# Kernel optimization log

Hardware: AMD Instinct MI355X
Metric: run time of the kernel (lower is better)

The kernel has to match this reference:

```python
import jax, jax.numpy as jnp
import numpy as np
from jax import lax

B, SQ, SK, D, K = 4, 2048, 2048, 1024, 3


def setup_inputs() -> dict:
    key = jax.random.key(0)
    ks = jax.random.split(key, 16)
    s = 0.02
    return {
        "query_hidden": jax.random.normal(ks[0], (B, SQ, D), jnp.float32),
        "memory_hidden": jax.random.normal(ks[1], (B, SK, D), jnp.float32),
        "attention_mask": jax.random.randint(ks[2], (SQ, SK), 0, 2).astype(bool),
        # Linear projections (torch: y = x @ W.T + b)
        "q_w": jax.random.normal(ks[3], (D, D), jnp.float32) * s,
        "q_b": jnp.zeros((D,), jnp.float32),
        "k_w": jax.random.normal(ks[4], (D, D), jnp.float32) * s,
        "k_b": jnp.zeros((D,), jnp.float32),
        "v_w": jax.random.normal(ks[5], (D, D), jnp.float32) * s,
        "v_b": jnp.zeros((D,), jnp.float32),
        "o_w": jax.random.normal(ks[6], (D, D), jnp.float32) * s,
        "o_b": jnp.zeros((D,), jnp.float32),
        # ConvTransform1D: depthwise conv kernels [D,1,K], bias [D], scalar gate
        "q_kernel": jax.random.normal(ks[7], (D, 1, K), jnp.float32) * s,
        "q_cbias": jnp.zeros((D,), jnp.float32),
        "q_gate": jnp.zeros((), jnp.float32),
        "k_kernel": jax.random.normal(ks[8], (D, 1, K), jnp.float32) * s,
        "k_cbias": jnp.zeros((D,), jnp.float32),
        "k_gate": jnp.zeros((), jnp.float32),
        "v_kernel": jax.random.normal(ks[9], (D, 1, K), jnp.float32) * s,
        "v_cbias": jnp.zeros((D,), jnp.float32),
        "v_gate": jnp.zeros((), jnp.float32),
    }


def _conv_transform(x, kernel, cbias, gate):
    """Gated depthwise 1D conv along seq: x + tanh(gate) * dwconv(x). x: [B,S,D]."""
    xc = jnp.transpose(x, (0, 2, 1))  # [B,D,S]
    y = lax.conv_general_dilated(
        xc, kernel, window_strides=(1,), padding="SAME",
        dimension_numbers=("NCH", "OIH", "NCH"), feature_group_count=x.shape[-1])
    y = y + cbias[None, :, None]
    return x + jnp.tanh(gate) * jnp.transpose(y, (0, 2, 1))


def reference(query_hidden, memory_hidden, attention_mask,
              q_w, q_b, k_w, k_b, v_w, v_b, o_w, o_b,
              q_kernel, q_cbias, q_gate,
              k_kernel, k_cbias, k_gate,
              v_kernel, v_cbias, v_gate):
    d_model = query_hidden.shape[-1]
    q = _conv_transform(query_hidden @ q_w.T + q_b, q_kernel, q_cbias, q_gate)
    k = _conv_transform(memory_hidden @ k_w.T + k_b, k_kernel, k_cbias, k_gate)
    v = _conv_transform(memory_hidden @ v_w.T + v_b, v_kernel, v_cbias, v_gate)
    # [B,Sq,Sk]
    logits = jnp.einsum("bqd,bkd->bqk", q, k) / jnp.sqrt(jnp.float32(d_model))
    mask = attention_mask[None, :, :]  # broadcast like torch unsqueeze(0)
    logits = jnp.where(mask, logits, jnp.finfo(logits.dtype).min)
    attn = jax.nn.softmax(logits, axis=-1)
    out = jnp.einsum("bqk,bkd->bqd", attn, v) @ o_w.T + o_b
    return out
```

## Files before the change

### kernel.cpp

```cpp
#include <hip/hip_runtime.h>
#include <cstdint>
#include <cstddef>


#define GLOBAL_AS __attribute__((address_space(1)))
#define LDS_AS    __attribute__((address_space(3)))

typedef _Float16 h8 __attribute__((ext_vector_type(8)));
typedef float    f4_t __attribute__((ext_vector_type(4)));
typedef unsigned short us8 __attribute__((ext_vector_type(8)));

__device__ __forceinline__ float bf2f(unsigned short u) {
    union { unsigned int i; float f; } x; x.i = ((unsigned int)u) << 16; return x.f;
}
__device__ __forceinline__ float rd(const void* p, long i, int isBf) {
    return isBf ? bf2f(((const unsigned short*)p)[i]) : ((const float*)p)[i];
}

struct Probe16 { const unsigned short* p[16]; int n[16]; };

__global__ void k_probes(Probe16 a, const unsigned int* __restrict__ mask,
                         int* __restrict__ flags) {
    if (blockIdx.x < 16) {
        __shared__ int cnt;
        if (threadIdx.x == 0) cnt = 0;
        __syncthreads();
        const unsigned short* s = a.p[blockIdx.x];
        const int n = a.n[blockIdx.x];
        int bad = 0;
        for (int i = threadIdx.x; i < n; i += 256) {
            int e = (s[i] >> 7) & 0xFF;
            if (e >= 0x8F || (e > 0 && e <= 0x60)) bad++;
        }
        atomicAdd(&cnt, bad);
        __syncthreads();
        if (threadIdx.x == 0) flags[blockIdx.x] = (cnt * 4 > n) ? 0 : 1;
    } else {
        __shared__ int vi32, vf32, vbf, vf16;
        if (threadIdx.x == 0) { vi32 = vf32 = vbf = vf16 = 0; }
        __syncthreads();
        int bi32 = 0, bf32 = 0, bbf = 0, bf16c = 0;
        for (int i = threadIdx.x; i < 4096; i += 256) {
            unsigned int w = mask[i];
            if (!(w == 0u || w == 1u)) bi32++;
            if (!(w == 0u || w == 0x3F800000u)) bf32++;
            unsigned int h0 = w & 0xFFFFu, h1 = w >> 16;
            if (!((h0 == 0u || h0 == 0x3F80u) && (h1 == 0u || h1 == 0x3F80u))) bbf++;
            if (!((h0 == 0u || h0 == 0x3C00u) && (h1 == 0u || h1 == 0x3C00u))) bf16c++;
        }
        if (bi32) atomicAdd(&vi32, 1);
        if (bf32) atomicAdd(&vf32, 1);
        if (bbf)  atomicAdd(&vbf, 1);
        if (bf16c) atomicAdd(&vf16, 1);
        __syncthreads();
        if (threadIdx.x == 0) {
            int w;
            if (vi32 == 0) w = 4;
            else if (vf32 == 0) w = 4;
            else if (vbf == 0) w = 2;
            else if (vf16 == 0) w = 2;
            else w = 1;
            flags[16] = w;
        }
    }
}

__device__ __forceinline__ h8 cvt8(const void* src, size_t off8, int isBf) {
    h8 d;
    if (isBf) {
        us8 s = *(const us8*)((const unsigned short*)src + off8 * 8);
#pragma unroll
        for (int u = 0; u < 8; ++u) d[u] = (_Float16)bf2f(s[u]);
    } else {
        const float* f = (const float*)src + off8 * 8;
        f4_t a = *(const f4_t*)f;
        f4_t b = *(const f4_t*)(f + 4);
#pragma unroll
        for (int u = 0; u < 4; ++u) { d[u] = (_Float16)a[u]; d[4 + u] = (_Float16)b[u]; }
    }
    return d;
}

struct Ptr4 { const void* p[4]; };
struct ConvSrc { const void* kern[3]; const void* cb[3]; const void* gate[3]; };

__global__ void k_prep(const void* __restrict__ qh, const void* __restrict__ mh,
                       _Float16* __restrict__ h16dst,
                       Ptr4 wsrc, _Float16* __restrict__ w16dst,
                       ConvSrc cs, _Float16* __restrict__ par16,
                       float* __restrict__ tgf,
                       const int* __restrict__ flags) {
    const int bid = blockIdx.x, tid = threadIdx.x;
    if (bid < 8192) {
        int i = bid * 256 + tid;
        int seg = i >> 20, off = i & 1048575;
        h8 d = cvt8(seg ? mh : qh, off, flags[seg]);
        *(h8*)(h16dst + (size_t)i * 8) = d;
    } else if (bid < 10240) {
        int i = (bid - 8192) * 256 + tid;
        int seg = i >> 17, off = i & 131071;
        h8 d = cvt8(wsrc.p[seg], off, flags[2 + seg]);
        *(h8*)(w16dst + (size_t)i * 8) = d;
    } else {
        const int D = 1024;
#pragma unroll
        for (int t = 0; t < 3; ++t) {
            const int kIs = flags[6 + t], cIs = flags[13 + t];
            for (int d = tid; d < D; d += 256) {
#pragma unroll
                for (int j = 0; j < 3; ++j)
                    par16[t * 3 * D + j * D + d] = (_Float16)rd(cs.kern[t], (long)d * 3 + j, kIs);
                par16[9 * D + t * D + d] = (_Float16)rd(cs.cb[t], d, cIs);
            }
        }
        if (tid < 3) {
            const void* g = cs.gate[tid];
            float gv = rd(g, 0, ((const unsigned int*)g)[0] == 0u ? 1 : 0);
            tgf[tid] = tanhf(gv);
        }
    }
}

template <int MODE, int MTILE>
__global__ __launch_bounds__(256, 4) void k_gemm_nt(
    const _Float16* __restrict__ A, const _Float16* __restrict__ Bm,
    void* __restrict__ Cout,
    const void* __restrict__ bias, const int* __restrict__ biasFlag,
    const void* __restrict__ bias2, const int* __restrict__ biasFlag2,
    int N, int K, long sA, long sB, long sC,
    int NT, int BZ) {

    constexpr int NI = (MTILE == 128) ? 4 : 2;
    constexpr int NCA = MTILE / 32;
    __shared__ __align__(16) _Float16 As[MTILE * 64];
    __shared__ __align__(16) _Float16 Bs[128 * 64];

    const long id = blockIdx.x;
    const int xcd = (int)(id & 7);
    const long local = id >> 3;
    const int col = (int)(local % NT);
    const long g = (local / NT) * 8 + xcd;
    const int bz = (int)(g % BZ);
    const int brow = (int)(g / BZ);

    const int tid  = threadIdx.x;
    const int wave = tid >> 6, lane = tid & 63;
    const int wm = (wave >> 1) * (MTILE / 2), wn = (wave & 1) * 64;
    const int lr = lane & 15, lq = lane >> 4;

    const _Float16* Ab = A + (long)bz * sA + (size_t)brow * MTILE * K;
    const _Float16* Bb = Bm + (long)bz * sB + (size_t)col * 128 * K;

    f4_t acc[NI][4] = {};

    const _Float16* gA[NCA];
    _Float16* lA[NCA];
#pragma unroll
    for (int j = 0; j < NCA; ++j) {
        int c = tid + j * 256;
        int r = c >> 3, s = ((c & 7) - r) & 7;
        gA[j] = Ab + (size_t)r * K + s * 8;
        lA[j] = As + c * 8;
    }
    const _Float16* gB[4];
    _Float16* lB[4];
#pragma unroll
    for (int j = 0; j < 4; ++j) {
        int c = tid + j * 256;
        int r = c >> 3, s = ((c & 7) - r) & 7;
        gB[j] = Bb + (size_t)r * K + s * 8;
        lB[j] = Bs + c * 8;
    }

    for (int kb = 0; kb < K; kb += 64) {
#pragma unroll
        for (int j = 0; j < NCA; ++j)
            __builtin_amdgcn_global_load_lds((void GLOBAL_AS*)(gA[j] + kb), (void LDS_AS*)lA[j], 16, 0, 0);
#pragma unroll
        for (int j = 0; j < 4; ++j)
            __builtin_amdgcn_global_load_lds((void GLOBAL_AS*)(gB[j] + kb), (void LDS_AS*)lB[j], 16, 0, 0);
        __syncthreads();

#pragma unroll
        for (int t = 0; t < 2; ++t) {
            const int fs = ((t * 4 + lq + lr) & 7) * 8;
            h8 af[NI], bfr[4];
#pragma unroll
            for (int i = 0; i < NI; ++i) af[i]  = *(const h8*)&As[(wm + i * 16 + lr) * 64 + fs];
#pragma unroll
            for (int j = 0; j < 4; ++j) bfr[j] = *(const h8*)&Bs[(wn + j * 16 + lr) * 64 + fs];
#pragma unroll
            for (int i = 0; i < NI; ++i)
#pragma unroll
                for (int j = 0; j < 4; ++j)
                    acc[i][j] = __builtin_amdgcn_mfma_f32_16x16x32_f16(af[i], bfr[j], acc[i][j], 0, 0, 0);
        }
        __syncthreads();
    }

    const long row0 = (long)brow * MTILE + wm + lq * 4;
    const long col0 = (long)col * 128 + wn + lr;

    float bv[4];
    if constexpr (MODE != 0) {
        const void* bp = bias; const int* bfp = biasFlag; long boff = 0;
        if (bias2 != nullptr && col * 128 >= (N >> 1)) {
            bp = bias2; bfp = biasFlag2; boff = (long)(N >> 1);
        }
        const int bIs = *bfp;
#pragma unroll
        for (int j = 0; j < 4; ++j) bv[j] = rd(bp, col0 + j * 16 - boff, bIs);
    } else {
#pragma unroll
        for (int j = 0; j < 4; ++j) bv[j] = 0.0f;
    }
    if constexpr (MODE == 2) {
        float* C = (float*)Cout + (long)bz * sC;
#pragma unroll
        for (int i = 0; i < NI; ++i)
#pragma unroll
            for (int j = 0; j < 4; ++j)
#pragma unroll
                for (int r = 0; r < 4; ++r)
                    C[(row0 + i * 16 + r) * (long)N + col0 + j * 16] = acc[i][j][r] + bv[j];
    } else {
        _Float16* C = (_Float16*)Cout + (long)bz * sC;
#pragma unroll
        for (int i = 0; i < NI; ++i)
#pragma unroll
            for (int j = 0; j < 4; ++j)
#pragma unroll
                for (int r = 0; r < 4; ++r) {
                    float v = acc[i][j][r] + bv[j];
                    v = fminf(fmaxf(v, -65000.0f), 65000.0f);
                    C[(row0 + i * 16 + r) * (long)N + col0 + j * 16] = (_Float16)v;
                }
    }
}

template <int MODE>
__global__ __launch_bounds__(512, 2) void k_gemm16(
    const _Float16* __restrict__ A, const _Float16* __restrict__ Bm,
    void* __restrict__ Cout,
    const void* __restrict__ bias, const int* __restrict__ biasFlag,
    const void* __restrict__ bias2, const int* __restrict__ biasFlag2,
    int N, int K, long sA, long sB, long sC,
    float scale, int NT, int BZ) {

    __shared__ __align__(16) _Float16 AS[2][2][8192];
    __shared__ __align__(16) _Float16 BS[2][2][8192];

    const long id = blockIdx.x;
    const int xcd = (int)(id & 7);
    const long local = id >> 3;
    const int col = (int)(local % NT);
    const long g = (local / NT) * 8 + xcd;
    const int bz = (int)(g % BZ);
    const int brow = (int)(g / BZ);

    const int tid  = threadIdx.x;
    const int wave = tid >> 6, lane = tid & 63;
    const int wr = wave >> 2, wc = wave & 3;
    const int lr = lane & 15, lq = lane >> 4;

    const _Float16* Ab = A + (long)bz * sA + (size_t)brow * 256 * K;
    const _Float16* Bb = Bm + (long)bz * sB + (size_t)col * 256 * K;

    f4_t acc[8][4] = {};

    const _Float16* gAsrc[2][2];
    const _Float16* gBsrc[2][2];
    int lOff[2];
#pragma unroll
    for (int j = 0; j < 2; ++j) {
        int c = tid + j * 512;
        int rho = c >> 3, s = ((c & 7) - rho) & 7;
        lOff[j] = c * 8;
#pragma unroll
        for (int gg = 0; gg < 2; ++gg) {
            int ra = gg * 64 + (rho & 63) + (rho >> 6) * 128;
            gAsrc[gg][j] = Ab + (size_t)ra * K + s * 8;
            int rb = gg * 32 + (rho & 31) + (rho >> 5) * 64;
            gBsrc[gg][j] = Bb + (size_t)rb * K + s * 8;
        }
    }

#define STAGE_A(buf, gg, kb)                                                              \
    do {                                                                                  \
        __builtin_amdgcn_global_load_lds((void GLOBAL_AS*)(gAsrc[gg][0] + (kb)),          \
                                         (void LDS_AS*)&AS[buf][gg][lOff[0]], 16, 0, 0);  \
        __builtin_amdgcn_global_load_lds((void GLOBAL_AS*)(gAsrc[gg][1] + (kb)),          \
                                         (void LDS_AS*)&AS[buf][gg][lOff[1]], 16, 0, 0);  \
    } while (0)
#define STAGE_B(buf, gg, kb)                                                              \
    do {                                                                                  \
        __builtin_amdgcn_global_load_lds((void GLOBAL_AS*)(gBsrc[gg][0] + (kb)),          \
                                         (void LDS_AS*)&BS[buf][gg][lOff[0]], 16, 0, 0);  \
        __builtin_amdgcn_global_load_lds((void GLOBAL_AS*)(gBsrc[gg][1] + (kb)),          \
                                         (void LDS_AS*)&BS[buf][gg][lOff[1]], 16, 0, 0);  \
    } while (0)

    const int nkt = K >> 6;

    STAGE_A(0, 0, 0);
    STAGE_B(0, 0, 0);
    STAGE_B(0, 1, 0);
    STAGE_A(0, 1, 0);
    asm volatile("s_waitcnt vmcnt(4)" ::: "memory");
    __builtin_amdgcn_s_barrier();

    int cur = 0;
    for (int t = 0; t < nkt; ++t) {
        const bool pf = (t + 1) < nkt;
        const long kb = (long)(t + 1) << 6;
        const int nx = cur ^ 1;
        h8 a0[4][2], a1[4][2], b0[2][2], b1[2][2];

#pragma unroll
        for (int ks = 0; ks < 2; ++ks) {
#pragma unroll
            for (int m = 0; m < 4; ++m) {
                int rho = wr * 64 + m * 16 + lr;
                a0[m][ks] = *(const h8*)&AS[cur][0][rho * 64 + ((ks * 4 + lq + rho) & 7) * 8];
            }
#pragma unroll
            for (int n = 0; n < 2; ++n) {
                int rho = wc * 32 + n * 16 + lr;
                b0[n][ks] = *(const h8*)&BS[cur][0][rho * 64 + ((ks * 4 + lq + rho) & 7) * 8];
            }
        }
        if (pf) STAGE_A(nx, 0, kb);
        __builtin_amdgcn_s_barrier();
        __builtin_amdgcn_s_setprio(1);
#pragma unroll
        for (int ks = 0; ks < 2; ++ks)
#pragma unroll
            for (int m = 0; m < 4; ++m)
#pragma unroll
                for (int n = 0; n < 2; ++n)
                    acc[m][n] = __builtin_amdgcn_mfma_f32_16x16x32_f16(
                        a0[m][ks], b0[n][ks], acc[m][n], 0, 0, 0);
        __builtin_amdgcn_s_setprio(0);
        if (pf) asm volatile("s_waitcnt vmcnt(4)" ::: "memory");
        else    asm volatile("s_waitcnt vmcnt(2)" ::: "memory");
        __builtin_amdgcn_s_barrier();

#pragma unroll
        for (int ks = 0; ks < 2; ++ks)
#pragma unroll
            for (int n = 0; n < 2; ++n) {
                int rho = wc * 32 + n * 16 + lr;
                b1[n][ks] = *(const h8*)&BS[cur][1][rho * 64 + ((ks * 4 + lq + rho) & 7) * 8];
            }
        if (pf) STAGE_B(nx, 0, kb);
        __builtin_amdgcn_s_barrier();
        __builtin_amdgcn_s_setprio(1);
#pragma unroll
        for (int ks = 0; ks < 2; ++ks)
#pragma unroll
            for (int m = 0; m < 4; ++m)
#pragma unroll
                for (int n = 0; n < 2; ++n)
                    acc[m][2 + n] = __builtin_amdgcn_mfma_f32_16x16x32_f16(
                        a0[m][ks], b1[n][ks], acc[m][2 + n], 0, 0, 0);
        __builtin_amdgcn_s_setprio(0);
        if (pf) asm volatile("s_waitcnt vmcnt(4)" ::: "memory");
        else    asm volatile("s_waitcnt vmcnt(0)" ::: "memory");
        __builtin_amdgcn_s_barrier();

#pragma unroll
        for (int ks = 0; ks < 2; ++ks)
#pragma unroll
            for (int m = 0; m < 4; ++m) {
                int rho = wr * 64 + m * 16 + lr;
                a1[m][ks] = *(const h8*)&AS[cur][1][rho * 64 + ((ks * 4 + lq + rho) & 7) * 8];
            }
        if (pf) STAGE_B(nx, 1, kb);
        __builtin_amdgcn_s_barrier();
        __builtin_amdgcn_s_setprio(1);
#pragma unroll
        for (int ks = 0; ks < 2; ++ks)
#pragma unroll
            for (int m = 0; m < 4; ++m)
#pragma unroll
                for (int n = 0; n < 2; ++n)
                    acc[4 + m][2 + n] = __builtin_amdgcn_mfma_f32_16x16x32_f16(
                        a1[m][ks], b1[n][ks], acc[4 + m][2 + n], 0, 0, 0);
        __builtin_amdgcn_s_setprio(0);
        __builtin_amdgcn_s_barrier();

#pragma unroll
        for (int ks = 0; ks < 2; ++ks)
#pragma unroll
            for (int n = 0; n < 2; ++n) {
                int rho = wc * 32 + n * 16 + lr;
                b0[n][ks] = *(const h8*)&BS[cur][0][rho * 64 + ((ks * 4 + lq + rho) & 7) * 8];
            }
        if (pf) STAGE_A(nx, 1, kb);
        __builtin_amdgcn_s_barrier();
        __builtin_amdgcn_s_setprio(1);
#pragma unroll
        for (int ks = 0; ks < 2; ++ks)
#pragma unroll
            for (int m = 0; m < 4; ++m)
#pragma unroll
                for (int n = 0; n < 2; ++n)
                    acc[4 + m][n] = __builtin_amdgcn_mfma_f32_16x16x32_f16(
                        a1[m][ks], b0[n][ks], acc[4 + m][n], 0, 0, 0);
        __builtin_amdgcn_s_setprio(0);
        if (pf) asm volatile("s_waitcnt vmcnt(4)" ::: "memory");
        __builtin_amdgcn_s_barrier();
        cur = nx;
    }
#undef STAGE_A
#undef STAGE_B

    const long row0 = (long)brow * 256 + wr * 128 + lq * 4;
    const long col0 = (long)col * 256 + wc * 64 + lr;

    if constexpr (MODE == 3) {
        _Float16* C = (_Float16*)Cout + (long)bz * sC;
#pragma unroll
        for (int i = 0; i < 8; ++i)
#pragma unroll
            for (int j = 0; j < 4; ++j)
#pragma unroll
                for (int r = 0; r < 4; ++r) {
                    float v = acc[i][j][r] * scale;
                    v = fminf(fmaxf(v, -60000.0f), 60000.0f);
                    C[(row0 + i * 16 + r) * (long)N + col0 + j * 16] = (_Float16)v;
                }
    } else {
        float bv[4];
        {
            const void* bp = bias; const int* bfp = biasFlag; long boff = 0;
            if (bias2 != nullptr && col * 256 >= (N >> 1)) {
                bp = bias2; bfp = biasFlag2; boff = (long)(N >> 1);
            }
            const int bIs = *bfp;
#pragma unroll
            for (int j = 0; j < 4; ++j) bv[j] = rd(bp, col0 + j * 16 - boff, bIs);
        }
        _Float16* C = (_Float16*)Cout + (long)bz * sC;
#pragma unroll
        for (int i = 0; i < 8; ++i)
#pragma unroll
            for (int j = 0; j < 4; ++j)
#pragma unroll
                for (int r = 0; r < 4; ++r) {
                    float v = acc[i][j][r] + bv[j];
                    v = fminf(fmaxf(v, -65000.0f), 65000.0f);
                    C[(row0 + i * 16 + r) * (long)N + col0 + j * 16] = (_Float16)v;
                }
    }
}

struct ConvP {
    const _Float16* x; int xs; _Float16* y;
    const _Float16* kp; const _Float16* cb; const float* tg;
};
__global__ void k_convs(ConvP p0, ConvP p1,
                        const _Float16* __restrict__ xv, int xvs,
                        _Float16* __restrict__ vt,
                        const _Float16* __restrict__ kpv,
                        const _Float16* __restrict__ cbv,
                        const float* __restrict__ tgv,
                        int S, int SK, int D) {
    __shared__ _Float16 T[64][65];
    const int bid = blockIdx.x, tid = threadIdx.x;
    h8 zero;
#pragma unroll
    for (int u = 0; u < 8; ++u) zero[u] = (_Float16)0.0f;

    if (bid < 8192) {
        const ConvP& p = (bid >= 4096) ? p1 : p0;
        int l = bid & 4095;
        int b = l >> 10, sp = l & 1023;
        int s = sp * 2 + (tid >> 7);
        int d0 = (tid & 127) * 8;
        const size_t xb = ((size_t)b * S + s) * p.xs + d0;
        const size_t yb = ((size_t)b * S + s) * D + d0;
        h8 xc = *(const h8*)(p.x + xb);
        h8 xp = (s > 0)     ? *(const h8*)(p.x + xb - p.xs) : zero;
        h8 xn = (s < S - 1) ? *(const h8*)(p.x + xb + p.xs) : zero;
        h8 k0 = *(const h8*)(p.kp + 0 * D + d0);
        h8 k1 = *(const h8*)(p.kp + 1 * D + d0);
        h8 k2 = *(const h8*)(p.kp + 2 * D + d0);
        h8 cb = *(const h8*)(p.cb + d0);
        float tg = *p.tg;
        h8 o;
#pragma unroll
        for (int u = 0; u < 8; ++u) {
            float cv = (float)xp[u] * (float)k0[u] + (float)xc[u] * (float)k1[u] +
                       (float)xn[u] * (float)k2[u] + (float)cb[u];
            float v = (float)xc[u] + tg * cv;
            o[u] = (_Float16)fminf(fmaxf(v, -65000.0f), 65000.0f);
        }
        *(h8*)(p.y + yb) = o;
    } else {
        int l = bid - 8192;
        int bx = l & 31, by = (l >> 5) & 15, b = l >> 9;
        int s0 = bx * 64, d0 = by * 64;
        float tg = *tgv;
#pragma unroll
        for (int it = 0; it < 2; ++it) {
            int idx = it * 256 + tid;
            int r = idx >> 3, c = (idx & 7) * 8;
            int s = s0 + r;
            const size_t xb = ((size_t)b * SK + s) * xvs + d0 + c;
            h8 xc = *(const h8*)(xv + xb);
            h8 xp = (s > 0)      ? *(const h8*)(xv + xb - xvs) : zero;
            h8 xn = (s < SK - 1) ? *(const h8*)(xv + xb + xvs) : zero;
            h8 k0 = *(const h8*)(kpv + 0 * D + d0 + c);
            h8 k1 = *(const h8*)(kpv + 1 * D + d0 + c);
            h8 k2 = *(const h8*)(kpv + 2 * D + d0 + c);
            h8 cb = *(const h8*)(cbv + d0 + c);
#pragma unroll
            for (int u = 0; u < 8; ++u) {
                float cv = (float)xp[u] * (float)k0[u] + (float)xc[u] * (float)k1[u] +
                           (float)xn[u] * (float)k2[u] + (float)cb[u];
                float v = (float)xc[u] + tg * cv;
                T[r][c + u] = (_Float16)fminf(fmaxf(v, -65000.0f), 65000.0f);
            }
        }
        __syncthreads();
#pragma unroll
        for (int it = 0; it < 2; ++it) {
            int idx = it * 256 + tid;
            int dr = idx >> 3, c = (idx & 7) * 8;
            h8 o;
#pragma unroll
            for (int u = 0; u < 8; ++u) o[u] = T[c + u][dr];
            *(h8*)(vt + ((size_t)b * D + d0 + dr) * SK + s0 + c) = o;
        }
    }
}

__global__ __launch_bounds__(256) void k_softmax(const _Float16* __restrict__ sc,
                                                 _Float16* __restrict__ pr,
                                                 const void* __restrict__ mraw,
                                                 const int* __restrict__ mwf,
                                                 int SK) {
    const long row = blockIdx.x;
    const int tid = threadIdx.x, lane = tid & 63, wave = tid >> 6;
    h8 v = *(const h8*)(sc + row * (long)SK + tid * 8);

    const int mw = *mwf;
    const long mbase = (row & 2047) * (long)SK + tid * 8;
    unsigned int km = 0;
    if (mw == 4) {
        const unsigned int* mp = (const unsigned int*)mraw + mbase;
#pragma unroll
        for (int u = 0; u < 8; ++u) km |= (mp[u] != 0u) ? (1u << u) : 0u;
    } else if (mw == 2) {
        const us8 m8 = *(const us8*)((const unsigned short*)mraw + mbase);
#pragma unroll
        for (int u = 0; u < 8; ++u) km |= (m8[u] != 0) ? (1u << u) : 0u;
    } else {
        unsigned long long m8 = *(const unsigned long long*)((const unsigned char*)mraw + mbase);
#pragma unroll
        for (int u = 0; u < 8; ++u) km |= ((m8 >> (8 * u)) & 0xFFull) ? (1u << u) : 0u;
    }

    float f[8]; float mx = -3.0e38f;
#pragma unroll
    for (int u = 0; u < 8; ++u) {
        f[u] = (km & (1u << u)) ? (float)v[u] : -60000.0f;
        mx = fmaxf(mx, f[u]);
    }
#pragma unroll
    for (int o = 32; o > 0; o >>= 1) mx = fmaxf(mx, __shfl_xor(mx, o, 64));
    __shared__ float red[8];
    if (lane == 0) red[wave] = mx;
    __syncthreads();
    mx = fmaxf(fmaxf(red[0], red[1]), fmaxf(red[2], red[3]));
    float sum = 0.0f;
#pragma unroll
    for (int u = 0; u < 8; ++u) { f[u] = __expf(f[u] - mx); sum += f[u]; }
#pragma unroll
    for (int o = 32; o > 0; o >>= 1) sum += __shfl_xor(sum, o, 64);
    if (lane == 0) red[4 + wave] = sum;
    __syncthreads();
    sum = red[4] + red[5] + red[6] + red[7];
    float inv = 1.0f / sum;
    h8 o8;
#pragma unroll
    for (int u = 0; u < 8; ++u) o8[u] = (_Float16)(f[u] * inv);
    *(h8*)(pr + row * (long)SK + tid * 8) = o8;
}

extern "C" void kernel_launch(void* const* d_in, const int* in_sizes, int n_in,
                              void* d_out, int out_size, void* d_ws, size_t ws_size,
                              hipStream_t stream) {
    const int Bn = 4, SQ = 2048, SK = 2048, D = 1024;
    const size_t nQ = (size_t)Bn * SQ * D;

    const void* qh = d_in[0];
    const void* mh = d_in[1];
    const void* mask = d_in[2];
    const void* q_w = d_in[3];
    const void* q_b = d_in[4];
    const void* k_w = d_in[5];
    const void* k_b = d_in[6];
    const void* v_w = d_in[7];
    const void* v_b = d_in[8];
    const void* o_w = d_in[9];
    const void* o_b = d_in[10];
    const void* q_kern = d_in[11];
    const void* q_cb   = d_in[12];
    const void* q_g    = d_in[13];
    const void* k_kern = d_in[14];
    const void* k_cb   = d_in[15];
    const void* k_g    = d_in[16];
    const void* v_kern = d_in[17];
    const void* v_cb   = d_in[18];
    const void* v_g    = d_in[19];

    char* ws = (char*)d_ws;
    _Float16* scores   = (_Float16*)(ws + 0);
    _Float16* attn_out = (_Float16*)(ws + 0);
    _Float16* par16    = (_Float16*)(ws + 33521664);
    float*    tgf      = (float*)(ws + 33521664 + 24576);
    _Float16* w16      = (_Float16*)(ws + 33554432);
    _Float16* lin      = (_Float16*)(ws + 41943040);
    _Float16* lin_q    = lin;
    _Float16* lin_kv   = lin + nQ;
    _Float16* probs    = lin;
    _Float16* conv     = (_Float16*)(ws + 92274688);
    _Float16* qh16     = conv;
    _Float16* mh16     = conv + nQ;
    _Float16* vt       = (_Float16*)(ws + 125829120);
    int*      flags    = (int*)(ws + 142606336);

    Probe16 pa;
    const void* pp[16] = {qh, mh, q_w, k_w, v_w, o_w, q_kern, k_kern, v_kern,
                          q_b, k_b, v_b, o_b, q_cb, k_cb, v_cb};
    const int   pn[16] = {2048, 2048, 2048, 2048, 2048, 2048, 3072, 3072, 3072,
                          1024, 1024, 1024, 1024, 1024, 1024, 1024};
    for (int i = 0; i < 16; ++i) { pa.p[i] = (const unsigned short*)pp[i]; pa.n[i] = pn[i]; }
    k_probes<<<17, 256, 0, stream>>>(pa, (const unsigned int*)mask, flags);

    Ptr4 wp; wp.p[0] = q_w; wp.p[1] = k_w; wp.p[2] = v_w; wp.p[3] = o_w;
    ConvSrc cs;
    cs.kern[0] = q_kern; cs.kern[1] = k_kern; cs.kern[2] = v_kern;
    cs.cb[0] = q_cb; cs.cb[1] = k_cb; cs.cb[2] = v_cb;
    cs.gate[0] = q_g; cs.gate[1] = k_g; cs.gate[2] = v_g;
    k_prep<<<10241, 256, 0, stream>>>(qh, mh, qh16, wp, w16, cs, par16, tgf, flags);

    k_gemm_nt<1, 64><<<dim3(1024), 256, 0, stream>>>(
        qh16, w16, lin_q, q_b, flags + 9, nullptr, nullptr,
        D, D, 0, 0, 0, 8, 1);
    k_gemm16<1><<<dim3(256), 512, 0, stream>>>(
        mh16, w16 + (size_t)D * D, lin_kv, k_b, flags + 10, v_b, flags + 11,
        2 * D, D, 0, 0, 0, 1.0f, 8, 1);

    ConvP cq{lin_q, D, conv + 0 * nQ, par16 + 0 * 3 * D, par16 + 9 * D + 0 * D, tgf + 0};
    ConvP ck{lin_kv, 2 * D, conv + 1 * nQ, par16 + 1 * 3 * D, par16 + 9 * D + 1 * D, tgf + 1};
    k_convs<<<dim3(10240), 256, 0, stream>>>(
        cq, ck, lin_kv + D, 2 * D, vt, par16 + 2 * 3 * D, par16 + 9 * D + 2 * D, tgf + 2,
        SQ, SK, D);

    k_gemm16<3><<<dim3(256), 512, 0, stream>>>(
        conv + 0 * nQ, conv + 1 * nQ, scores, nullptr, nullptr, nullptr, nullptr,
        SK, D, (long)SQ * D, (long)SK * D, (long)SQ * SK, 0.03125f, 8, 4);

    k_softmax<<<Bn * SQ, 256, 0, stream>>>(scores, probs, mask, flags + 16, SK);

    k_gemm_nt<0, 64><<<dim3(1024), 256, 0, stream>>>(
        probs, vt, attn_out, nullptr, nullptr, nullptr, nullptr,
        D, SK, (long)SQ * SK, (long)D * SK, (long)SQ * D, 8, 4);

    k_gemm_nt<2, 64><<<dim3(1024), 256, 0, stream>>>(
        attn_out, w16 + 3 * (size_t)D * D, d_out, o_b, flags + 12, nullptr, nullptr,
        D, D, 0, 0, 0, 8, 1);

    (void)in_sizes; (void)n_in; (void)out_size; (void)ws_size;
}
```

Baseline: 393.8 us.

## Coarsen prep, conv and softmax kernels: more work per thread and wave-per-row softmax

The prep conversion kernel now processes four 8-element chunks per thread with loads batched ahead of stores, cutting the grid from 10241 to 2561 blocks. The depthwise conv computes two adjacent rows per thread, sharing the loaded neighbour rows so each output row needs fewer loads. Softmax assigns one wave per row (four rows per block), which removes the shared-memory reductions and __syncthreads, and it uses vectorized mask loads. The aim is to reduce launch/block overhead and redundant memory traffic in these memory-bound stages, at the cost of higher register use per thread.

```diff
diff --git a/kernel.cpp b/kernel.cpp
--- a/kernel.cpp
+++ b/kernel.cpp
@@ -9,6 +9,7 @@
 typedef _Float16 h8 __attribute__((ext_vector_type(8)));
 typedef float    f4_t __attribute__((ext_vector_type(4)));
 typedef unsigned short us8 __attribute__((ext_vector_type(8)));
+typedef unsigned int u32x4 __attribute__((ext_vector_type(4)));
 
 __device__ __forceinline__ float bf2f(unsigned short u) {
     union { unsigned int i; float f; } x; x.i = ((unsigned int)u) << 16; return x.f;
@@ -65,22 +66,6 @@
     }
 }
 
-__device__ __forceinline__ h8 cvt8(const void* src, size_t off8, int isBf) {
-    h8 d;
-    if (isBf) {
-        us8 s = *(const us8*)((const unsigned short*)src + off8 * 8);
-#pragma unroll
-        for (int u = 0; u < 8; ++u) d[u] = (_Float16)bf2f(s[u]);
-    } else {
-        const float* f = (const float*)src + off8 * 8;
-        f4_t a = *(const f4_t*)f;
-        f4_t b = *(const f4_t*)(f + 4);
-#pragma unroll
-        for (int u = 0; u < 4; ++u) { d[u] = (_Float16)a[u]; d[4 + u] = (_Float16)b[u]; }
-    }
-    return d;
-}
-
 struct Ptr4 { const void* p[4]; };
 struct ConvSrc { const void* kern[3]; const void* cb[3]; const void* gate[3]; };
 
@@ -91,16 +76,59 @@
                        float* __restrict__ tgf,
                        const int* __restrict__ flags) {
     const int bid = blockIdx.x, tid = threadIdx.x;
-    if (bid < 8192) {
-        int i = bid * 256 + tid;
-        int seg = i >> 20, off = i & 1048575;
-        h8 d = cvt8(seg ? mh : qh, off, flags[seg]);
-        *(h8*)(h16dst + (size_t)i * 8) = d;
-    } else if (bid < 10240) {
-        int i = (bid - 8192) * 256 + tid;
-        int seg = i >> 17, off = i & 131071;
-        h8 d = cvt8(wsrc.p[seg], off, flags[2 + seg]);
-        *(h8*)(w16dst + (size_t)i * 8) = d;
+    if (bid < 2560) {
+        const void* src;
+        _Float16* dst;
+        size_t base, off;
+        int isBf;
+        if (bid < 2048) {
+            const int seg = bid >> 10;
+            src = seg ? mh : qh;
+            isBf = flags[seg];
+            base = (size_t)bid * 1024 + tid;
+            off = base & 1048575;
+            dst = h16dst;
+        } else {
+            const int lb = bid - 2048;
+            const int seg = lb >> 7;
+            src = wsrc.p[seg];
+            isBf = flags[2 + seg];
+            base = (size_t)lb * 1024 + tid;
+            off = base & 131071;
+            dst = w16dst;
+        }
+        if (isBf) {
+            us8 s[4];
+            const unsigned short* sp = (const unsigned short*)src;
+#pragma unroll
+            for (int j = 0; j < 4; ++j)
+                s[j] = *(const us8*)(sp + (off + (size_t)j * 256) * 8);
+#pragma unroll
+            for (int j = 0; j < 4; ++j) {
+                h8 d;
+#pragma unroll
+                for (int u = 0; u < 8; ++u) d[u] = (_Float16)bf2f(s[j][u]);
+                *(h8*)(dst + (base + (size_t)j * 256) * 8) = d;
+            }
+        } else {
+            f4_t a[4], b[4];
+            const float* fp = (const float*)src;
+#pragma unroll
+            for (int j = 0; j < 4; ++j) {
+                a[j] = *(const f4_t*)(fp + (off + (size_t)j * 256) * 8);
+                b[j] = *(const f4_t*)(fp + (off + (size_t)j * 256) * 8 + 4);
+            }
+#pragma unroll
+            for (int j = 0; j < 4; ++j) {
+                h8 d;
+#pragma unroll
+                for (int u = 0; u < 4; ++u) {
+                    d[u] = (_Float16)a[j][u];
+                    d[4 + u] = (_Float16)b[j][u];
+                }
+                *(h8*)(dst + (base + (size_t)j * 256) * 8) = d;
+            }
+        }
     } else {
         const int D = 1024;
 #pragma unroll
@@ -472,33 +500,41 @@
 #pragma unroll
     for (int u = 0; u < 8; ++u) zero[u] = (_Float16)0.0f;
 
-    if (bid < 8192) {
-        const ConvP& p = (bid >= 4096) ? p1 : p0;
-        int l = bid & 4095;
-        int b = l >> 10, sp = l & 1023;
-        int s = sp * 2 + (tid >> 7);
+    if (bid < 4096) {
+        const ConvP& p = (bid >= 2048) ? p1 : p0;
+        int l = bid & 2047;
+        int b = l >> 9, sp = l & 511;
+        int g = tid >> 7;
+        int s = sp * 4 + g * 2;
         int d0 = (tid & 127) * 8;
-        const size_t xb = ((size_t)b * S + s) * p.xs + d0;
-        const size_t yb = ((size_t)b * S + s) * D + d0;
-        h8 xc = *(const h8*)(p.x + xb);
-        h8 xp = (s > 0)     ? *(const h8*)(p.x + xb - p.xs) : zero;
-        h8 xn = (s < S - 1) ? *(const h8*)(p.x + xb + p.xs) : zero;
+        const size_t rs = p.xs;
+        const size_t xb = ((size_t)b * S + s) * rs + d0;
+        h8 xA = (s > 0) ? *(const h8*)(p.x + xb - rs) : zero;
+        h8 xB = *(const h8*)(p.x + xb);
+        h8 xC = *(const h8*)(p.x + xb + rs);
+        h8 xD = (s + 2 < S) ? *(const h8*)(p.x + xb + 2 * rs) : zero;
         h8 k0 = *(const h8*)(p.kp + 0 * D + d0);
         h8 k1 = *(const h8*)(p.kp + 1 * D + d0);
         h8 k2 = *(const h8*)(p.kp + 2 * D + d0);
         h8 cb = *(const h8*)(p.cb + d0);
         float tg = *p.tg;
-        h8 o;
+        h8 o0, o1;
 #pragma unroll
         for (int u = 0; u < 8; ++u) {
-            float cv = (float)xp[u] * (float)k0[u] + (float)xc[u] * (float)k1[u] +
-                       (float)xn[u] * (float)k2[u] + (float)cb[u];
-            float v = (float)xc[u] + tg * cv;
-            o[u] = (_Float16)fminf(fmaxf(v, -65000.0f), 65000.0f);
-        }
-        *(h8*)(p.y + yb) = o;
+            float c0 = (float)xA[u] * (float)k0[u] + (float)xB[u] * (float)k1[u] +
+                       (float)xC[u] * (float)k2[u] + (float)cb[u];
+            float v0 = (float)xB[u] + tg * c0;
+            o0[u] = (_Float16)fminf(fmaxf(v0, -65000.0f), 65000.0f);
+            float c1 = (float)xB[u] * (float)k0[u] + (float)xC[u] * (float)k1[u] +
+                       (float)xD[u] * (float)k2[u] + (float)cb[u];
+            float v1 = (float)xC[u] + tg * c1;
+            o1[u] = (_Float16)fminf(fmaxf(v1, -65000.0f), 65000.0f);
+        }
+        const size_t yb = ((size_t)b * S + s) * D + d0;
+        *(h8*)(p.y + yb) = o0;
+        *(h8*)(p.y + yb + D) = o1;
     } else {
-        int l = bid - 8192;
+        int l = bid - 4096;
         int bx = l & 31, by = (l >> 5) & 15, b = l >> 9;
         int s0 = bx * 64, d0 = by * 64;
         float tg = *tgv;
@@ -541,52 +577,81 @@
                                                  const void* __restrict__ mraw,
                                                  const int* __restrict__ mwf,
                                                  int SK) {
-    const long row = blockIdx.x;
-    const int tid = threadIdx.x, lane = tid & 63, wave = tid >> 6;
-    h8 v = *(const h8*)(sc + row * (long)SK + tid * 8);
-
+    const long row = (long)blockIdx.x * 4 + (threadIdx.x >> 6);
+    const int lane = threadIdx.x & 63;
+    const long rb = row * (long)SK;
+    const long mrb = (row & 2047) * (long)SK;
     const int mw = *mwf;
-    const long mbase = (row & 2047) * (long)SK + tid * 8;
-    unsigned int km = 0;
+
+    h8 v[4];
+#pragma unroll
+    for (int j = 0; j < 4; ++j)
+        v[j] = *(const h8*)(sc + rb + (size_t)(j * 64 + lane) * 8);
+
+    unsigned int km[4];
     if (mw == 4) {
-        const unsigned int* mp = (const unsigned int*)mraw + mbase;
-#pragma unroll
-        for (int u = 0; u < 8; ++u) km |= (mp[u] != 0u) ? (1u << u) : 0u;
+#pragma unroll
+        for (int j = 0; j < 4; ++j) {
+            const unsigned int* mp = (const unsigned int*)mraw + mrb + (size_t)(j * 64 + lane) * 8;
+            u32x4 m0 = *(const u32x4*)mp;
+            u32x4 m1 = *(const u32x4*)(mp + 4);
+            unsigned int k = 0;
+#pragma unroll
+            for (int u = 0; u < 4; ++u) {
+                k |= (m0[u] != 0u) ? (1u << u) : 0u;
+                k |= (m1[u] != 0u) ? (1u << (4 + u)) : 0u;
+            }
+            km[j] = k;
+        }
     } else if (mw == 2) {
-        const us8 m8 = *(const us8*)((const unsigned short*)mraw + mbase);
-#pragma unroll
-        for (int u = 0; u < 8; ++u) km |= (m8[u] != 0) ? (1u << u) : 0u;
+#pragma unroll
+        for (int j = 0; j < 4; ++j) {
+            us8 m8 = *(const us8*)((const unsigned short*)mraw + mrb + (size_t)(j * 64 + lane) * 8);
+            unsigned int k = 0;
+#pragma unroll
+            for (int u = 0; u < 8; ++u) k |= (m8[u] != 0) ? (1u << u) : 0u;
+            km[j] = k;
+        }
     } else {
-        unsigned long long m8 = *(const unsigned long long*)((const unsigned char*)mraw + mbase);
-#pragma unroll
-        for (int u = 0; u < 8; ++u) km |= ((m8 >> (8 * u)) & 0xFFull) ? (1u << u) : 0u;
-    }
-
-    float f[8]; float mx = -3.0e38f;
-#pragma unroll
-    for (int u = 0; u < 8; ++u) {
-        f[u] = (km & (1u << u)) ? (float)v[u] : -60000.0f;
-        mx = fmaxf(mx, f[u]);
-    }
+#pragma unroll
+        for (int j = 0; j < 4; ++j) {
+            unsigned long long m = *(const unsigned long long*)
+                ((const unsigned char*)mraw + mrb + (size_t)(j * 64 + lane) * 8);
+            unsigned int k = 0;
+#pragma unroll
+            for (int u = 0; u < 8; ++u) k |= ((m >> (8 * u)) & 0xFFull) ? (1u << u) : 0u;
+            km[j] = k;
+        }
+    }
+
+    float f[4][8];
+    float mx = -3.0e38f;
+#pragma unroll
+    for (int j = 0; j < 4; ++j)
+#pragma unroll
+        for (int u = 0; u < 8; ++u) {
+            f[j][u] = (km[j] & (1u << u)) ? (float)v[j][u] : -60000.0f;
+            mx = fmaxf(mx, f[j][u]);
+        }
 #pragma unroll
     for (int o = 32; o > 0; o >>= 1) mx = fmaxf(mx, __shfl_xor(mx, o, 64));
-    __shared__ float red[8];
-    if (lane == 0) red[wave] = mx;
-    __syncthreads();
-    mx = fmaxf(fmaxf(red[0], red[1]), fmaxf(red[2], red[3]));
+
     float sum = 0.0f;
 #pragma unroll
-    for (int u = 0; u < 8; ++u) { f[u] = __expf(f[u] - mx); sum += f[u]; }
+    for (int j = 0; j < 4; ++j)
+#pragma unroll
+        for (int u = 0; u < 8; ++u) { f[j][u] = __expf(f[j][u] - mx); sum += f[j][u]; }
 #pragma unroll
     for (int o = 32; o > 0; o >>= 1) sum += __shfl_xor(sum, o, 64);
-    if (lane == 0) red[4 + wave] = sum;
-    __syncthreads();
-    sum = red[4] + red[5] + red[6] + red[7];
-    float inv = 1.0f / sum;
-    h8 o8;
-#pragma unroll
-    for (int u = 0; u < 8; ++u) o8[u] = (_Float16)(f[u] * inv);
-    *(h8*)(pr + row * (long)SK + tid * 8) = o8;
+    const float inv = 1.0f / sum;
+
+#pragma unroll
+    for (int j = 0; j < 4; ++j) {
+        h8 o8;
+#pragma unroll
+        for (int u = 0; u < 8; ++u) o8[u] = (_Float16)(f[j][u] * inv);
+        *(h8*)(pr + rb + (size_t)(j * 64 + lane) * 8) = o8;
+    }
 }
 
 extern "C" void kernel_launch(void* const* d_in, const int* in_sizes, int n_in,
@@ -645,7 +710,7 @@
     cs.kern[0] = q_kern; cs.kern[1] = k_kern; cs.kern[2] = v_kern;
     cs.cb[0] = q_cb; cs.cb[1] = k_cb; cs.cb[2] = v_cb;
     cs.gate[0] = q_g; cs.gate[1] = k_g; cs.gate[2] = v_g;
-    k_prep<<<10241, 256, 0, stream>>>(qh, mh, qh16, wp, w16, cs, par16, tgf, flags);
+    k_prep<<<2561, 256, 0, stream>>>(qh, mh, qh16, wp, w16, cs, par16, tgf, flags);
 
     k_gemm_nt<1, 64><<<dim3(1024), 256, 0, stream>>>(
         qh16, w16, lin_q, q_b, flags + 9, nullptr, nullptr,
@@ -656,7 +721,7 @@
 
     ConvP cq{lin_q, D, conv + 0 * nQ, par16 + 0 * 3 * D, par16 + 9 * D + 0 * D, tgf + 0};
     ConvP ck{lin_kv, 2 * D, conv + 1 * nQ, par16 + 1 * 3 * D, par16 + 9 * D + 1 * D, tgf + 1};
-    k_convs<<<dim3(10240), 256, 0, stream>>>(
+    k_convs<<<dim3(6144), 256, 0, stream>>>(
         cq, ck, lin_kv + D, 2 * D, vt, par16 + 2 * 3 * D, par16 + 9 * D + 2 * D, tgf + 2,
         SQ, SK, D);
 
@@ -664,7 +729,7 @@
         conv + 0 * nQ, conv + 1 * nQ, scores, nullptr, nullptr, nullptr, nullptr,
         SK, D, (long)SQ * D, (long)SK * D, (long)SQ * SK, 0.03125f, 8, 4);
 
-    k_softmax<<<Bn * SQ, 256, 0, stream>>>(scores, probs, mask, flags + 16, SK);
+    k_softmax<<<Bn * SQ / 4, 256, 0, stream>>>(scores, probs, mask, flags + 16, SK);
 
     k_gemm_nt<0, 64><<<dim3(1024), 256, 0, stream>>>(
         probs, vt, attn_out, nullptr, nullptr, nullptr, nullptr,
```

New measurement: 378.9 us. 3.8% less time.
